# Performance work log

Measured on AMD Instinct MI355X. Metric: run time of the kernel, lower is better.

## Reference

```python
import jax, jax.numpy as jnp
import numpy as np

V = 32000   # vocab.size
E = 512     # embed_dim
H = 512     # hidden_dim
L = 2       # num_layers
W = 32      # window_size
S = 512     # seq_len
B = 8       # batch


def setup_inputs() -> dict:
    key = jax.random.key(0)
    ks = jax.random.split(key, 2 + 4 * L)
    bound = 1.0 / np.sqrt(H)
    inp = {
        "encoder_input": jax.random.randint(ks[0], (S, B), 0, V),
        "embed_table": jax.random.normal(ks[1], (V, E), jnp.float32),
    }
    for l in range(L):
        in_dim = E if l == 0 else H
        k = ks[2 + 4 * l: 6 + 4 * l]
        inp[f"w_ih_{l}"] = jax.random.uniform(k[0], (4 * H, in_dim), jnp.float32, -bound, bound)
        inp[f"w_hh_{l}"] = jax.random.uniform(k[1], (4 * H, H), jnp.float32, -bound, bound)
        inp[f"b_ih_{l}"] = jax.random.uniform(k[2], (4 * H,), jnp.float32, -bound, bound)
        inp[f"b_hh_{l}"] = jax.random.uniform(k[3], (4 * H,), jnp.float32, -bound, bound)
    return inp


def _lstm_layer(x, mask, w_ih, w_hh, b_ih, b_hh):
    # x: [T, N, D]; mask: [T, N, 1]. Masked steps keep (h, c), so every window
    # effectively starts from a zero state at its first valid position (same as
    # running a fresh LSTM on each window, torch gate order i,f,g,o).
    N = x.shape[1]
    Hd = w_hh.shape[1]
    bias = b_ih + b_hh

    def step(carry, inp_):
        h, c = carry
        xt, mt = inp_
        gates = xt @ w_ih.T + h @ w_hh.T + bias  # [N, 4H]
        i, f, g, o = jnp.split(gates, 4, axis=-1)
        i = jax.nn.sigmoid(i)
        f = jax.nn.sigmoid(f)
        g = jnp.tanh(g)
        o = jax.nn.sigmoid(o)
        c_new = f * c + i * g
        h_new = o * jnp.tanh(c_new)
        h = jnp.where(mt, h_new, h)
        c = jnp.where(mt, c_new, c)
        return (h, c), h

    z = jnp.zeros((N, Hd), x.dtype)
    (h, _), ys = jax.lax.scan(step, (z, z), (x, mask))
    return ys, h


def reference(encoder_input, embed_table,
              w_ih_0, w_hh_0, b_ih_0, b_hh_0,
              w_ih_1, w_hh_1, b_ih_1, b_hh_1):
    emb = embed_table[encoder_input]              # [S, B, E]
    T = W + 1
    # window position t for target index i is i - W + t (invalid when < 0)
    pos = jnp.arange(S)[None, :] - W + jnp.arange(T)[:, None]  # [T, S]
    valid = pos >= 0
    windows = emb[jnp.clip(pos, 0)]               # [T, S, B, E]
    x = windows.reshape(T, S * B, E)
    mask = jnp.broadcast_to(valid[:, :, None], (T, S, B)).reshape(T, S * B, 1)

    params = [(w_ih_0, w_hh_0, b_ih_0, b_hh_0), (w_ih_1, w_hh_1, b_ih_1, b_hh_1)]
    h = None
    for (wi, wh, bi, bh) in params:
        x, h = _lstm_layer(x, mask, wi, wh, bi, bh)
    # original takes encoder_output at the last window position == final hidden
    return h.reshape(S, B, H)
```

## Files before the change

### kernel.cpp

```cpp
#include <hip/hip_runtime.h>
#include <stdint.h>

#define NROWS 4096
#define HDIM  512
#define GDIM  2048
#define WWIN  32

typedef __attribute__((ext_vector_type(8))) short short8;
typedef __attribute__((ext_vector_type(4))) float f32x4;

__device__ __forceinline__ unsigned short f2bf(float x){
  union { float f; unsigned int u; } v; v.f = x;
  unsigned int u = v.u + 0x7fffu + ((v.u >> 16) & 1u);
  return (unsigned short)(u >> 16);
}
__device__ __forceinline__ float bf2f(unsigned short u){
  union { unsigned int u; float f; } v; v.u = ((unsigned int)u) << 16; return v.f;
}

__device__ __forceinline__ void gld16(const void* g, void* l){
  __builtin_amdgcn_global_load_lds(
      (const __attribute__((address_space(1))) unsigned int*)g,
      (__attribute__((address_space(3))) unsigned int*)l, 16, 0, 0);
}

__device__ __forceinline__ float sigm(float x){ return 1.f/(1.f + __expf(-x)); }
__device__ __forceinline__ float tanh_f(float x){ return 1.f - 2.f/(1.f + __expf(2.f*x)); }

__device__ __forceinline__ void grid_sync(unsigned* bar, unsigned target){
  __syncthreads();
  if (threadIdx.x == 0){
    unsigned arrived = __hip_atomic_fetch_add(&bar[0], 1u, __ATOMIC_RELAXED,
                                              __HIP_MEMORY_SCOPE_AGENT);
    if (arrived == gridDim.x - 1){
      __hip_atomic_store(&bar[0], 0u, __ATOMIC_RELAXED, __HIP_MEMORY_SCOPE_AGENT);
      __hip_atomic_store(&bar[1], target, __ATOMIC_RELAXED, __HIP_MEMORY_SCOPE_AGENT);
    } else {
      while (__hip_atomic_load(&bar[1], __ATOMIC_RELAXED, __HIP_MEMORY_SCOPE_AGENT) < target)
        __builtin_amdgcn_s_sleep(8);
    }
  }
  asm volatile("" ::: "memory");
  __syncthreads();
}

__device__ __forceinline__ void gemm_tile_db(
    const char* A0, const char* A1, const char* Bsrc,
    int ldbB, int nk, int r0, int c0,
    char* smem, int wr, int wc, int lane, f32x4 acc[4][4])
{
  const int tid = threadIdx.x;
  const int oo0 = tid * 16;
  const int srow = oo0 >> 7;
  const int scb  = oo0 & 127;
  const size_t aOff = (size_t)(r0 + srow) * 1024 + scb;
  const size_t bOff = (size_t)(c0 + srow) * (size_t)ldbB + scb;

  auto STAGE = [&](int kk, int buf){
    const char* Ap = (kk < 8) ? A0 : A1;
    const size_t kbA = (size_t)(kk & 7) * 128;
    const size_t kbB = (size_t)kk * 128;
    char* AsB = smem + buf * 16384;
    char* BsB = smem + 32768 + buf * 16384;
    #pragma unroll
    for (int i = 0; i < 4; ++i){
      const size_t rstep = (size_t)i * 32;
      gld16(Ap   + aOff + rstep * 1024          + kbA, AsB + i*4096 + oo0);
      gld16(Bsrc + bOff + rstep * (size_t)ldbB  + kbB, BsB + i*4096 + oo0);
    }
  };

  STAGE(0, 0);
  __syncthreads();

  const int lr = lane & 15;
  const int lk = (lane >> 4) * 8;

  for (int kk = 0; kk < nk; ++kk){
    const int cur = kk & 1;
    if (kk + 1 < nk) STAGE(kk + 1, cur ^ 1);

    const unsigned short* As = (const unsigned short*)(smem + cur*16384);
    const unsigned short* Bs = (const unsigned short*)(smem + 32768 + cur*16384);
    short8 a[2][4], b[2][4];
    #pragma unroll
    for (int h = 0; h < 2; ++h){
      const int k32 = h * 32;
      #pragma unroll
      for (int m = 0; m < 4; ++m)
        a[h][m] = *(const short8*)(As + (64*wr + 16*m + lr)*64 + k32 + lk);
      #pragma unroll
      for (int n = 0; n < 4; ++n)
        b[h][n] = *(const short8*)(Bs + (64*wc + 16*n + lr)*64 + k32 + lk);
    }
    __builtin_amdgcn_s_setprio(1);
    #pragma unroll
    for (int h = 0; h < 2; ++h)
      #pragma unroll
      for (int m = 0; m < 4; ++m)
        #pragma unroll
        for (int n = 0; n < 4; ++n)
          acc[m][n] = __builtin_amdgcn_mfma_f32_16x16x32_bf16(a[h][m], b[h][n], acc[m][n], 0, 0, 0);
    __builtin_amdgcn_s_setprio(0);

    __syncthreads();
  }
}

__global__ void __launch_bounds__(256) prep_weights(
    const float* wih0, const float* whh0, const float* bih0, const float* bhh0,
    const float* wih1, const float* whh1, const float* bih1, const float* bhh1,
    unsigned short* BrIh0, unsigned short* Br0, unsigned short* Br1,
    float* bias0r, float* br1)
{
  const int j = blockIdx.x;
  const int g = j & 3, hd = j >> 2;
  const int r = g*512 + hd;
  for (int k = threadIdx.x; k < 512; k += 256){
    BrIh0[(size_t)j*512 + k]      = f2bf(wih0[(size_t)r*512 + k]);
    Br0  [(size_t)j*512 + k]      = f2bf(whh0[(size_t)r*512 + k]);
    Br1  [(size_t)j*1024 + k]     = f2bf(wih1[(size_t)r*512 + k]);
    Br1  [(size_t)j*1024 + 512+k] = f2bf(whh1[(size_t)r*512 + k]);
  }
  if (threadIdx.x == 0){
    bias0r[j] = bih0[r] + bhh0[r];
    br1[j]    = bih1[r] + bhh1[r];
  }
}

__global__ void __launch_bounds__(256) gather_embed(const int* enc, const float* tbl,
                                                    unsigned short* E)
{
  const int n = blockIdx.x;
  const int idx = enc[n];
  const float* src = tbl + (size_t)idx * 512;
  unsigned short* dst = E + (size_t)n * 512;
  for (int e = threadIdx.x; e < 512; e += 256) dst[e] = f2bf(src[e]);
}

__global__ void __launch_bounds__(256) p0_gemm(const unsigned short* E,
                                               const unsigned short* BrIh0,
                                               const float* bias0r,
                                               unsigned short* P0)
{
  __shared__ __align__(16) char smem[65536];
  const int tid  = threadIdx.x;
  const int lane = tid & 63, wid = tid >> 6;
  const int wr = wid >> 1, wc = wid & 1;
  const int bid = blockIdx.x;
  const int r0 = (bid >> 4) * 128, c0 = (bid & 15) * 128;
  f32x4 acc[4][4] = {};
  gemm_tile_db((const char*)E, nullptr, (const char*)BrIh0, 1024, 8,
               r0, c0, smem, wr, wc, lane, acc);
  #pragma unroll
  for (int m = 0; m < 4; ++m){
    const int rowb = r0 + 64*wr + 16*m + ((lane >> 4) << 2);
    #pragma unroll
    for (int n = 0; n < 4; ++n){
      const int colb = c0 + 64*wc + 16*n + (lane & 15);
      const float bs = bias0r[colb];
      #pragma unroll
      for (int r = 0; r < 4; ++r)
        P0[(size_t)(rowb + r)*GDIM + colb] = f2bf(acc[m][n][r] + bs);
    }
  }
}

__global__ void __launch_bounds__(512, 2) persist_kernel(
    unsigned short* h0, unsigned short* h1,
    const unsigned short* Br0, const unsigned short* Br1,
    const unsigned short* P0, const float* br1, float* out, unsigned* bar)
{
  extern __shared__ __align__(16) char smem[];

  const int bid = blockIdx.x;
  const int x = bid & 7, i = bid >> 3;
  const bool L1 = (i & 1);
  const int rowg = (x >> 1) * 4 + ((i >> 1) & 3);
  const int colg = (x & 1) * 4 + ((i >> 3) & 3);
  const int r0  = rowg * 256;
  const int c0v = colg * 256;

  const int tid  = threadIdx.x;
  const int lane = tid & 63, wid = tid >> 6;
  const int wm = wid >> 2, wn = wid & 3;
  const int lr = lane & 15, sl = lane >> 4;
  const int ph = (sl ^ ((lr >> 1) & 3)) << 4;

  const int srowB  = tid >> 2;
  const int sbyteB = ((tid & 3) ^ ((tid >> 3) & 3)) << 4;
  const int ar   = tid >> 1;
  const int as0  = (tid & 1) * 2;
  const int akey = (ar >> 1) & 3;

  const char* Bp  = (const char*)(L1 ? Br1 : Br0);
  const int  ldbB = L1 ? 2048 : 1024;
  const int  nkt  = L1 ? 32 : 16;

  float creg[4][4][2];
  #pragma unroll
  for (int p = 0; p < 4; ++p)
    #pragma unroll
    for (int q = 0; q < 4; ++q){ creg[p][q][0] = 0.f; creg[p][q][1] = 0.f; }

  for (int tau = 0; tau <= 33; ++tau){
    const bool active = L1 ? (tau >= 1) : (tau <= 32);
    if (active){
      const int t  = L1 ? (tau - 1) : tau;
      const int pr = (tau + 1) & 1, pw = tau & 1;
      const unsigned short* hA0 = h0 + (size_t)pr * (NROWS*HDIM);
      const unsigned short* hA1 = h1 + (size_t)pr * (NROWS*HDIM);

      auto issueB = [&](int kt2){
        const char* s0 = Bp + (size_t)(c0v + srowB) * (size_t)ldbB + kt2*64 + sbyteB;
        char* d = smem + 32768 + (size_t)(kt2 & 3) * 16384 + tid * 16;
        gld16(s0, d);
        gld16(s0 + (size_t)128 * (size_t)ldbB, d + 8192);
      };
      auto issueA = [&](int kt2, unsigned long long a[4]){
        const unsigned short* hs; int kE;
        if (!L1 || kt2 < 16){ hs = hA0; kE = kt2 * 32; }
        else                { hs = hA1; kE = (kt2 - 16) * 32; }
        unsigned long long* p = (unsigned long long*)(hs + (size_t)(r0 + ar) * 512 + kE + as0 * 8);
        a[0] = __hip_atomic_load(p+0, __ATOMIC_RELAXED, __HIP_MEMORY_SCOPE_AGENT);
        a[1] = __hip_atomic_load(p+1, __ATOMIC_RELAXED, __HIP_MEMORY_SCOPE_AGENT);
        a[2] = __hip_atomic_load(p+2, __ATOMIC_RELAXED, __HIP_MEMORY_SCOPE_AGENT);
        a[3] = __hip_atomic_load(p+3, __ATOMIC_RELAXED, __HIP_MEMORY_SCOPE_AGENT);
      };
      auto writeA = [&](int kt2, const unsigned long long a[4]){
        char* base = smem + (size_t)(kt2 & 1) * 16384 + ar * 64;
        char* p0 = base + ((as0 ^ akey) << 4);
        char* p1 = base + (((as0 + 1) ^ akey) << 4);
        *(unsigned long long*)(p0)     = a[0];
        *(unsigned long long*)(p0 + 8) = a[1];
        *(unsigned long long*)(p1)     = a[2];
        *(unsigned long long*)(p1 + 8) = a[3];
      };

      f32x4 acc[8][4] = {};
      unsigned long long areg[4];

      issueA(0, areg);
      issueB(0); issueB(1);
      asm volatile("s_waitcnt vmcnt(4)" ::: "memory");
      writeA(0, areg);
      issueA(1, areg);
      asm volatile("s_waitcnt vmcnt(4)" ::: "memory");
      asm volatile("s_waitcnt lgkmcnt(0)" ::: "memory");
      __builtin_amdgcn_s_barrier();

      for (int kt = 0; kt < nkt; ++kt){
        const char* Ab = smem + (size_t)(kt & 1) * 16384;
        const char* Bb = smem + 32768 + (size_t)(kt & 3) * 16384;
        short8 a[8], b[4];
        #pragma unroll
        for (int m = 0; m < 8; ++m)
          a[m] = *(const short8*)(Ab + (wm*128 + m*16 + lr)*64 + ph);
        #pragma unroll
        for (int n = 0; n < 4; ++n)
          b[n] = *(const short8*)(Bb + (wn*64 + n*16 + lr)*64 + ph);

        const bool stB = (kt + 2) < nkt;
        if (stB) issueB(kt + 2);

        __builtin_amdgcn_s_setprio(1);
        #pragma unroll
        for (int m = 0; m < 8; ++m)
          #pragma unroll
          for (int n = 0; n < 4; ++n)
            acc[m][n] = __builtin_amdgcn_mfma_f32_16x16x32_bf16(a[m], b[n], acc[m][n], 0, 0, 0);
        __builtin_amdgcn_s_setprio(0);

        if (stB) asm volatile("s_waitcnt vmcnt(2)" ::: "memory");
        else     asm volatile("s_waitcnt vmcnt(0)" ::: "memory");
        if (kt + 1 < nkt){
          writeA(kt + 1, areg);
          if (kt + 2 < nkt) issueA(kt + 2, areg);
        }
        asm volatile("s_waitcnt lgkmcnt(0)" ::: "memory");
        __builtin_amdgcn_s_barrier();
      }

      float* GLDS = (float*)smem;
      const int GST = 68;
      unsigned short* hw = (L1 ? h1 : h0) + (size_t)pw * (NROWS*HDIM);
      const bool finalStep = (L1 && t == 32);
      const int cbase = c0v >> 2;

      #pragma unroll
      for (int pass = 0; pass < 4; ++pass){
        __syncthreads();
        if (wn == pass){
          #pragma unroll
          for (int m = 0; m < 8; ++m){
            const int rowb = wm*128 + m*16 + (sl << 2);
            #pragma unroll
            for (int n = 0; n < 4; ++n){
              const int colb = n*16 + lr;
              const f32x4 v = acc[m][n];
              #pragma unroll
              for (int r = 0; r < 4; ++r)
                GLDS[(rowb + r)*GST + colb] = v[r];
            }
          }
        }
        __syncthreads();
        #pragma unroll
        for (int it = 0; it < 4; ++it){
          const int pid = it*512 + tid;
          const int row = pid >> 3;
          const int pl  = (pid & 7) * 2;
          const int rowg = r0 + row;
          const int hd0  = cbase + pass*16 + pl;
          const float* gp = &GLDS[row*GST + 4*pl];
          const float4 g0 = *(const float4*)gp;
          const float4 g1 = *(const float4*)(gp + 4);
          float gi0 = g0.x, gf0 = g0.y, gg0 = g0.z, go0 = g0.w;
          float gi1 = g1.x, gf1 = g1.y, gg1 = g1.z, go1 = g1.w;
          const int s  = rowg >> 3;
          const int bb = rowg & 7;
          const int pos = s - WWIN + t;
          if (!L1){
            const int p0r = (pos < 0 ? 0 : pos)*8 + bb;
            const uint4 pv = *(const uint4*)&P0[(size_t)p0r*GDIM + 4*hd0];
            gi0 += bf2f((unsigned short)(pv.x & 0xffff));
            gf0 += bf2f((unsigned short)(pv.x >> 16));
            gg0 += bf2f((unsigned short)(pv.y & 0xffff));
            go0 += bf2f((unsigned short)(pv.y >> 16));
            gi1 += bf2f((unsigned short)(pv.z & 0xffff));
            gf1 += bf2f((unsigned short)(pv.z >> 16));
            gg1 += bf2f((unsigned short)(pv.w & 0xffff));
            go1 += bf2f((unsigned short)(pv.w >> 16));
          } else {
            const float4 b0 = *(const float4*)&br1[4*hd0];
            const float4 b1 = *(const float4*)&br1[4*hd0 + 4];
            gi0 += b0.x; gf0 += b0.y; gg0 += b0.z; go0 += b0.w;
            gi1 += b1.x; gf1 += b1.y; gg1 += b1.z; go1 += b1.w;
          }
          float cp0 = creg[pass][it][0];
          float cp1 = creg[pass][it][1];
          float i0 = sigm(gi0), f0 = sigm(gf0), gA = tanh_f(gg0), o0 = sigm(go0);
          float i1 = sigm(gi1), f1 = sigm(gf1), gB = tanh_f(gg1), o1 = sigm(go1);
          float cn0 = f0*cp0 + i0*gA;
          float cn1 = f1*cp1 + i1*gB;
          float hn0 = o0*tanh_f(cn0);
          float hn1 = o1*tanh_f(cn1);
          if (pos < 0){ cn0 = 0.f; hn0 = 0.f; cn1 = 0.f; hn1 = 0.f; }
          creg[pass][it][0] = cn0;
          creg[pass][it][1] = cn1;
          const size_t sidx0 = (size_t)rowg*HDIM + hd0;
          if (finalStep){
            *(float2*)&out[sidx0] = make_float2(hn0, hn1);
          } else {
            const unsigned hp = (unsigned)f2bf(hn0) | ((unsigned)f2bf(hn1) << 16);
            __hip_atomic_store((unsigned*)&hw[sidx0], hp, __ATOMIC_RELAXED,
                               __HIP_MEMORY_SCOPE_AGENT);
          }
        }
      }
    }
    if (tau != 33) grid_sync(bar, (unsigned)(tau + 1));
  }
}

__global__ void __launch_bounds__(512, 2) step_kernel(
    unsigned short* h0, unsigned short* h1, float* c0b, float* c1b,
    const unsigned short* Br0, const unsigned short* Br1,
    const unsigned short* P0, const float* br1, float* out, int tau, int bidOff)
{
  extern __shared__ __align__(16) char smem[];

  const int x = blockIdx.x & 7, kq = blockIdx.x >> 3;
  int wk;
  if (gridDim.x == 256) wk = ((kq & 1) << 7) + x * 16 + (kq >> 1);
  else                  wk = x * 16 + kq;
  wk += bidOff;

  const bool L1 = (wk >= 128);
  const int t  = L1 ? (tau - 1) : tau;
  const int pr = (tau + 1) & 1, pw = tau & 1;
  const int lb = L1 ? (wk - 128) : wk;
  const int r0  = (lb >> 3) * 256;
  const int c0v = (lb & 7) * 256;

  const int tid  = threadIdx.x;
  const int lane = tid & 63;
  const int wid  = tid >> 6;
  const int wm = wid >> 2, wn = wid & 3;
  const int lr = lane & 15, sl = lane >> 4;

  const unsigned short* hA0 = h0 + (size_t)pr * (NROWS*HDIM);
  const unsigned short* hA1 = h1 + (size_t)pr * (NROWS*HDIM);
  const char* Bp  = (const char*)(L1 ? Br1 : Br0);
  const int  ldbB = L1 ? 2048 : 1024;
  const int  nkt  = L1 ? 32 : 16;

  const int srow  = tid >> 2;
  const int sbyte = ((tid & 3) ^ ((tid >> 3) & 3)) << 4;
  const int ph    = (sl ^ ((lr >> 1) & 3)) << 4;
  const int laneA = (wm*128 + lr) * 64 + ph;
  const int laneB = (wn*64  + lr) * 64 + ph;

  auto STAGE_A = [&](int kt2, int c){
    const char* Ap; int kB;
    if (!L1 || kt2 < 16){ Ap = (const char*)hA0; kB = kt2 * 64; }
    else                { Ap = (const char*)hA1; kB = (kt2 - 16) * 64; }
    gld16(Ap + (size_t)(r0 + c*128 + srow) * 1024 + kB + sbyte,
          smem + (size_t)(kt2 & 3) * 32768 + c*8192 + tid*16);
  };
  auto STAGE_B = [&](int kt2, int c){
    gld16(Bp + (size_t)(c0v + c*128 + srow) * (size_t)ldbB + kt2*64 + sbyte,
          smem + (size_t)(kt2 & 3) * 32768 + 16384 + c*8192 + tid*16);
  };

  f32x4 acc[8][4] = {};

  STAGE_A(0,0); STAGE_A(0,1); STAGE_B(0,0); STAGE_B(0,1);
  STAGE_A(1,0); STAGE_A(1,1); STAGE_B(1,0); STAGE_B(1,1);
  asm volatile("s_waitcnt vmcnt(4)" ::: "memory");
  __builtin_amdgcn_s_barrier();

  for (int kt = 0; kt < nkt; ++kt){
    const char* bufp = smem + (size_t)(kt & 3) * 32768;
    const bool st = (kt + 2) < nkt;
    short8 a0[4], a1[4], b[4];

    #pragma unroll
    for (int m = 0; m < 4; ++m) a0[m] = *(const short8*)(bufp + laneA + m*1024);
    #pragma unroll
    for (int n = 0; n < 4; ++n) b[n]  = *(const short8*)(bufp + 16384 + laneB + n*1024);
    if (st){ STAGE_A(kt+2, 0); STAGE_A(kt+2, 1); }
    __builtin_amdgcn_s_barrier();
    asm volatile("s_waitcnt lgkmcnt(0)" ::: "memory");
    __builtin_amdgcn_sched_barrier(0);
    __builtin_amdgcn_s_setprio(1);
    #pragma unroll
    for (int m = 0; m < 4; ++m)
      #pragma unroll
      for (int n = 0; n < 4; ++n)
        acc[m][n] = __builtin_amdgcn_mfma_f32_16x16x32_bf16(a0[m], b[n], acc[m][n], 0, 0, 0);
    __builtin_amdgcn_s_setprio(0);
    __builtin_amdgcn_s_barrier();

    #pragma unroll
    for (int m = 0; m < 4; ++m) a1[m] = *(const short8*)(bufp + laneA + (4+m)*1024);
    if (st){
      STAGE_B(kt+2, 0); STAGE_B(kt+2, 1);
      asm volatile("s_waitcnt vmcnt(4)" ::: "memory");
    } else {
      asm volatile("s_waitcnt vmcnt(0)" ::: "memory");
    }
    __builtin_amdgcn_s_barrier();
    asm volatile("s_waitcnt lgkmcnt(0)" ::: "memory");
    __builtin_amdgcn_sched_barrier(0);
    __builtin_amdgcn_s_setprio(1);
    #pragma unroll
    for (int m = 0; m < 4; ++m)
      #pragma unroll
      for (int n = 0; n < 4; ++n)
        acc[4+m][n] = __builtin_amdgcn_mfma_f32_16x16x32_bf16(a1[m], b[n], acc[4+m][n], 0, 0, 0);
    __builtin_amdgcn_s_setprio(0);
    __builtin_amdgcn_s_barrier();
  }

  float* GLDS = (float*)smem;
  const int GST = 68;
  float* cbuf = L1 ? c1b : c0b;
  unsigned short* hw = (L1 ? h1 : h0) + (size_t)pw * (NROWS*HDIM);
  const bool finalStep = (L1 && t == 32);

  for (int pass = 0; pass < 4; ++pass){
    __syncthreads();
    if (wn == pass){
      #pragma unroll
      for (int m = 0; m < 8; ++m){
        const int rowb = wm*128 + m*16 + (sl << 2);
        #pragma unroll
        for (int n = 0; n < 4; ++n){
          const int colb = n*16 + lr;
          const f32x4 v = acc[m][n];
          #pragma unroll
          for (int r = 0; r < 4; ++r)
            GLDS[(rowb + r)*GST + colb] = v[r];
        }
      }
    }
    __syncthreads();
    #pragma unroll
    for (int it = 0; it < 8; ++it){
      const int cid = it*512 + tid;
      const int row = cid >> 4;
      const int l   = cid & 15;
      const int rowg = r0 + row;
      const int hd   = (c0v >> 2) + pass*16 + l;
      float4 gv = *(const float4*)&GLDS[row*GST + 4*l];
      float gi = gv.x, gf = gv.y, gg = gv.z, go = gv.w;
      const int s  = rowg >> 3;
      const int bb = rowg & 7;
      const int pos = s - WWIN + t;
      if (!L1){
        const int p0r = (pos < 0 ? 0 : pos)*8 + bb;
        const ushort4 pv = *(const ushort4*)&P0[(size_t)p0r*GDIM + 4*hd];
        gi += bf2f(pv.x); gf += bf2f(pv.y); gg += bf2f(pv.z); go += bf2f(pv.w);
      } else {
        float4 bv = *(const float4*)&br1[4*hd];
        gi += bv.x; gf += bv.y; gg += bv.z; go += bv.w;
      }
      const size_t sidx = (size_t)rowg*HDIM + hd;
      float cp = cbuf[sidx];
      float i_ = sigm(gi), f_ = sigm(gf), g_ = tanh_f(gg), o_ = sigm(go);
      float cn = f_*cp + i_*g_;
      float hn = o_*tanh_f(cn);
      if (pos < 0){ cn = 0.f; hn = 0.f; }
      cbuf[sidx] = cn;
      if (finalStep) out[sidx] = hn;
      else           hw[sidx]  = f2bf(hn);
    }
  }
}

extern "C" void kernel_launch(void* const* d_in, const int* in_sizes, int n_in,
                              void* d_out, int out_size, void* d_ws, size_t ws_size,
                              hipStream_t stream)
{
  const int*   enc  = (const int*)d_in[0];
  const float* tbl  = (const float*)d_in[1];
  const float* wih0 = (const float*)d_in[2];
  const float* whh0 = (const float*)d_in[3];
  const float* bih0 = (const float*)d_in[4];
  const float* bhh0 = (const float*)d_in[5];
  const float* wih1 = (const float*)d_in[6];
  const float* whh1 = (const float*)d_in[7];
  const float* bih1 = (const float*)d_in[8];
  const float* bhh1 = (const float*)d_in[9];
  float* out = (float*)d_out;

  char* ws = (char*)d_ws;
  size_t off = 0;
  auto alloc = [&](size_t bytes){
    char* p = ws + off; off += (bytes + 255) & ~(size_t)255; return p;
  };
  unsigned short* E     = (unsigned short*)alloc((size_t)NROWS*512*2);
  unsigned short* BrIh0 = (unsigned short*)alloc((size_t)GDIM*512*2);
  unsigned short* Br0   = (unsigned short*)alloc((size_t)GDIM*512*2);
  unsigned short* Br1   = (unsigned short*)alloc((size_t)GDIM*1024*2);
  float* bias0r = (float*)alloc(GDIM*4);
  float* br1    = (float*)alloc(GDIM*4);
  unsigned short* P0 = (unsigned short*)alloc((size_t)NROWS*GDIM*2);
  unsigned short* h0 = (unsigned short*)alloc((size_t)2*NROWS*HDIM*2);
  unsigned short* h1 = (unsigned short*)alloc((size_t)2*NROWS*HDIM*2);
  float* c0 = (float*)alloc((size_t)NROWS*HDIM*4);
  float* c1 = (float*)alloc((size_t)NROWS*HDIM*4);
  unsigned* bar = (unsigned*)alloc(256);
  if (off > ws_size) return;

  (void)hipFuncSetAttribute(reinterpret_cast<const void*>(persist_kernel),
                            hipFuncAttributeMaxDynamicSharedMemorySize, 98304);
  (void)hipFuncSetAttribute(reinterpret_cast<const void*>(step_kernel),
                            hipFuncAttributeMaxDynamicSharedMemorySize, 131072);

  hipMemsetAsync(h0, 0, (size_t)33554688, stream);

  prep_weights<<<2048, 256, 0, stream>>>(wih0, whh0, bih0, bhh0,
                                         wih1, whh1, bih1, bhh1,
                                         BrIh0, Br0, Br1, bias0r, br1);
  gather_embed<<<4096, 256, 0, stream>>>(enc, tbl, E);
  p0_gemm<<<512, 256, 0, stream>>>(E, BrIh0, bias0r, P0);

  int occ = 0;
  hipError_t oe = hipOccupancyMaxActiveBlocksPerMultiprocessor(
      &occ, reinterpret_cast<const void*>(persist_kernel), 512, 98304);
  bool coop = (oe == hipSuccess && occ >= 1);
  if (coop){
    void* kargs[] = {&h0, &h1, &Br0, &Br1, &P0, &br1, &out, &bar};
    hipError_t le = hipLaunchCooperativeKernel(
        reinterpret_cast<const void*>(persist_kernel),
        dim3(256), dim3(512), kargs, 98304, stream);
    if (le != hipSuccess) coop = false;
  }
  if (!coop){
    for (int tau = 0; tau <= 33; ++tau){
      const int grid = (tau == 0 || tau == 33) ? 128 : 256;
      const int boff = (tau == 33) ? 128 : 0;
      step_kernel<<<grid, 512, 131072, stream>>>(h0, h1, c0, c1, Br0, Br1,
                                                 P0, br1, out, tau, boff);
    }
  }
}
```

Measured before the change: 1.739 ms.

## Split persistent LSTM grid into 512 smaller blocks with per-row-band barriers

The persistent kernel now launches 512 blocks of 256 threads, each owning a 128-row by 256-column tile instead of 256-row by 256-column tiles, with smaller LDS buffers. The global grid barrier is replaced by a counter per 128-row band, so only the 16 blocks that share a band of hidden rows wait for each other at each timestep. This is meant to cut barrier latency and use more CUs for the recurrent GEMM. In exchange, B-matrix tiles go from triple-buffered to double-buffered and each block does more loads per unit of compute. The cooperative launch path also now requires an occupancy of 2 blocks per CU.

Measured after the change: 1.738 ms. Within noise of the previous version (-0.1%).

```diff
diff --git a/kernel.cpp b/kernel.cpp
--- a/kernel.cpp
+++ b/kernel.cpp
@@ -27,18 +27,12 @@
 __device__ __forceinline__ float sigm(float x){ return 1.f/(1.f + __expf(-x)); }
 __device__ __forceinline__ float tanh_f(float x){ return 1.f - 2.f/(1.f + __expf(2.f*x)); }
 
-__device__ __forceinline__ void grid_sync(unsigned* bar, unsigned target){
+__device__ __forceinline__ void band_sync(unsigned* ctr, unsigned target){
   __syncthreads();
   if (threadIdx.x == 0){
-    unsigned arrived = __hip_atomic_fetch_add(&bar[0], 1u, __ATOMIC_RELAXED,
-                                              __HIP_MEMORY_SCOPE_AGENT);
-    if (arrived == gridDim.x - 1){
-      __hip_atomic_store(&bar[0], 0u, __ATOMIC_RELAXED, __HIP_MEMORY_SCOPE_AGENT);
-      __hip_atomic_store(&bar[1], target, __ATOMIC_RELAXED, __HIP_MEMORY_SCOPE_AGENT);
-    } else {
-      while (__hip_atomic_load(&bar[1], __ATOMIC_RELAXED, __HIP_MEMORY_SCOPE_AGENT) < target)
-        __builtin_amdgcn_s_sleep(8);
-    }
+    __hip_atomic_fetch_add(ctr, 1u, __ATOMIC_RELAXED, __HIP_MEMORY_SCOPE_AGENT);
+    while (__hip_atomic_load(ctr, __ATOMIC_RELAXED, __HIP_MEMORY_SCOPE_AGENT) < target)
+      __builtin_amdgcn_s_sleep(2);
   }
   asm volatile("" ::: "memory");
   __syncthreads();
@@ -166,28 +160,27 @@
   }
 }
 
-__global__ void __launch_bounds__(512, 2) persist_kernel(
+__global__ void __launch_bounds__(256, 2) persist_kernel(
     unsigned short* h0, unsigned short* h1,
     const unsigned short* Br0, const unsigned short* Br1,
     const unsigned short* P0, const float* br1, float* out, unsigned* bar)
 {
   extern __shared__ __align__(16) char smem[];
 
-  const int bid = blockIdx.x;
-  const int x = bid & 7, i = bid >> 3;
-  const bool L1 = (i & 1);
-  const int rowg = (x >> 1) * 4 + ((i >> 1) & 3);
-  const int colg = (x & 1) * 4 + ((i >> 3) & 3);
-  const int r0  = rowg * 256;
-  const int c0v = colg * 256;
+  const int bid  = blockIdx.x;
+  const int colg = bid & 7;
+  const int bl   = bid >> 3;
+  const bool L1  = (bl & 1);
+  const int rb   = bl >> 1;
+  const int r0   = rb * 128;
+  const int c0v  = colg * 256;
 
   const int tid  = threadIdx.x;
   const int lane = tid & 63, wid = tid >> 6;
-  const int wm = wid >> 2, wn = wid & 3;
+  const int wn = wid;
   const int lr = lane & 15, sl = lane >> 4;
   const int ph = (sl ^ ((lr >> 1) & 3)) << 4;
 
-  const int srowB  = tid >> 2;
   const int sbyteB = ((tid & 3) ^ ((tid >> 3) & 3)) << 4;
   const int ar   = tid >> 1;
   const int as0  = (tid & 1) * 2;
@@ -196,6 +189,8 @@
   const char* Bp  = (const char*)(L1 ? Br1 : Br0);
   const int  ldbB = L1 ? 2048 : 1024;
   const int  nkt  = L1 ? 32 : 16;
+
+  unsigned* ctr = bar + rb * 32;
 
   float creg[4][4][2];
   #pragma unroll
@@ -212,23 +207,26 @@
       const unsigned short* hA1 = h1 + (size_t)pr * (NROWS*HDIM);
 
       auto issueB = [&](int kt2){
-        const char* s0 = Bp + (size_t)(c0v + srowB) * (size_t)ldbB + kt2*64 + sbyteB;
-        char* d = smem + 32768 + (size_t)(kt2 & 3) * 16384 + tid * 16;
-        gld16(s0, d);
-        gld16(s0 + (size_t)128 * (size_t)ldbB, d + 8192);
+        char* d = smem + 16384 + (size_t)(kt2 & 1) * 16384 + tid * 16;
+        const char* s = Bp + (size_t)(c0v + (tid >> 2)) * (size_t)ldbB
+                           + kt2 * 64 + sbyteB;
+        #pragma unroll
+        for (int i = 0; i < 4; ++i)
+          gld16(s + (size_t)(i * 64) * (size_t)ldbB, d + i * 4096);
       };
       auto issueA = [&](int kt2, unsigned long long a[4]){
         const unsigned short* hs; int kE;
         if (!L1 || kt2 < 16){ hs = hA0; kE = kt2 * 32; }
         else                { hs = hA1; kE = (kt2 - 16) * 32; }
-        unsigned long long* p = (unsigned long long*)(hs + (size_t)(r0 + ar) * 512 + kE + as0 * 8);
+        const unsigned long long* p =
+            (const unsigned long long*)(hs + (size_t)(r0 + ar) * 512 + kE + as0 * 8);
         a[0] = __hip_atomic_load(p+0, __ATOMIC_RELAXED, __HIP_MEMORY_SCOPE_AGENT);
         a[1] = __hip_atomic_load(p+1, __ATOMIC_RELAXED, __HIP_MEMORY_SCOPE_AGENT);
         a[2] = __hip_atomic_load(p+2, __ATOMIC_RELAXED, __HIP_MEMORY_SCOPE_AGENT);
         a[3] = __hip_atomic_load(p+3, __ATOMIC_RELAXED, __HIP_MEMORY_SCOPE_AGENT);
       };
       auto writeA = [&](int kt2, const unsigned long long a[4]){
-        char* base = smem + (size_t)(kt2 & 1) * 16384 + ar * 64;
+        char* base = smem + (size_t)(kt2 & 1) * 8192 + ar * 64;
         char* p0 = base + ((as0 ^ akey) << 4);
         char* p1 = base + (((as0 + 1) ^ akey) << 4);
         *(unsigned long long*)(p0)     = a[0];
@@ -241,8 +239,7 @@
       unsigned long long areg[4];
 
       issueA(0, areg);
-      issueB(0); issueB(1);
-      asm volatile("s_waitcnt vmcnt(4)" ::: "memory");
+      issueB(0);
       writeA(0, areg);
       issueA(1, areg);
       asm volatile("s_waitcnt vmcnt(4)" ::: "memory");
@@ -250,18 +247,16 @@
       __builtin_amdgcn_s_barrier();
 
       for (int kt = 0; kt < nkt; ++kt){
-        const char* Ab = smem + (size_t)(kt & 1) * 16384;
-        const char* Bb = smem + 32768 + (size_t)(kt & 3) * 16384;
+        if (kt + 1 < nkt) issueB(kt + 1);
+        const char* Ab = smem + (size_t)(kt & 1) * 8192;
+        const char* Bb = smem + 16384 + (size_t)(kt & 1) * 16384;
         short8 a[8], b[4];
-        #pragma unroll
-        for (int m = 0; m < 8; ++m)
-          a[m] = *(const short8*)(Ab + (wm*128 + m*16 + lr)*64 + ph);
         #pragma unroll
         for (int n = 0; n < 4; ++n)
           b[n] = *(const short8*)(Bb + (wn*64 + n*16 + lr)*64 + ph);
-
-        const bool stB = (kt + 2) < nkt;
-        if (stB) issueB(kt + 2);
+        #pragma unroll
+        for (int m = 0; m < 8; ++m)
+          a[m] = *(const short8*)(Ab + (m*16 + lr)*64 + ph);
 
         __builtin_amdgcn_s_setprio(1);
         #pragma unroll
@@ -271,14 +266,17 @@
             acc[m][n] = __builtin_amdgcn_mfma_f32_16x16x32_bf16(a[m], b[n], acc[m][n], 0, 0, 0);
         __builtin_amdgcn_s_setprio(0);
 
-        if (stB) asm volatile("s_waitcnt vmcnt(2)" ::: "memory");
-        else     asm volatile("s_waitcnt vmcnt(0)" ::: "memory");
         if (kt + 1 < nkt){
           writeA(kt + 1, areg);
-          if (kt + 2 < nkt) issueA(kt + 2, areg);
+          if (kt + 2 < nkt){
+            issueA(kt + 2, areg);
+            asm volatile("s_waitcnt vmcnt(4)" ::: "memory");
+          } else {
+            asm volatile("s_waitcnt vmcnt(0)" ::: "memory");
+          }
+          asm volatile("s_waitcnt lgkmcnt(0)" ::: "memory");
+          __builtin_amdgcn_s_barrier();
         }
-        asm volatile("s_waitcnt lgkmcnt(0)" ::: "memory");
-        __builtin_amdgcn_s_barrier();
       }
 
       float* GLDS = (float*)smem;
@@ -293,7 +291,7 @@
         if (wn == pass){
           #pragma unroll
           for (int m = 0; m < 8; ++m){
-            const int rowb = wm*128 + m*16 + (sl << 2);
+            const int rowb = m*16 + (sl << 2);
             #pragma unroll
             for (int n = 0; n < 4; ++n){
               const int colb = n*16 + lr;
@@ -307,7 +305,7 @@
         __syncthreads();
         #pragma unroll
         for (int it = 0; it < 4; ++it){
-          const int pid = it*512 + tid;
+          const int pid = it*256 + tid;
           const int row = pid >> 3;
           const int pl  = (pid & 7) * 2;
           const int rowg = r0 + row;
@@ -359,7 +357,7 @@
         }
       }
     }
-    if (tau != 33) grid_sync(bar, (unsigned)(tau + 1));
+    if (tau != 33) band_sync(ctr, 16u * (unsigned)(tau + 1));
   }
 }
 
@@ -551,15 +549,15 @@
   unsigned short* h1 = (unsigned short*)alloc((size_t)2*NROWS*HDIM*2);
   float* c0 = (float*)alloc((size_t)NROWS*HDIM*4);
   float* c1 = (float*)alloc((size_t)NROWS*HDIM*4);
-  unsigned* bar = (unsigned*)alloc(256);
+  unsigned* bar = (unsigned*)alloc(4096);
   if (off > ws_size) return;
 
   (void)hipFuncSetAttribute(reinterpret_cast<const void*>(persist_kernel),
-                            hipFuncAttributeMaxDynamicSharedMemorySize, 98304);
+                            hipFuncAttributeMaxDynamicSharedMemorySize, 65536);
   (void)hipFuncSetAttribute(reinterpret_cast<const void*>(step_kernel),
                             hipFuncAttributeMaxDynamicSharedMemorySize, 131072);
 
-  hipMemsetAsync(h0, 0, (size_t)33554688, stream);
+  hipMemsetAsync(h0, 0, (size_t)33558528, stream);
 
   prep_weights<<<2048, 256, 0, stream>>>(wih0, whh0, bih0, bhh0,
                                          wih1, whh1, bih1, bhh1,
@@ -569,13 +567,13 @@
 
   int occ = 0;
   hipError_t oe = hipOccupancyMaxActiveBlocksPerMultiprocessor(
-      &occ, reinterpret_cast<const void*>(persist_kernel), 512, 98304);
-  bool coop = (oe == hipSuccess && occ >= 1);
+      &occ, reinterpret_cast<const void*>(persist_kernel), 256, 49152);
+  bool coop = (oe == hipSuccess && occ >= 2);
   if (coop){
     void* kargs[] = {&h0, &h1, &Br0, &Br1, &P0, &br1, &out, &bar};
     hipError_t le = hipLaunchCooperativeKernel(
         reinterpret_cast<const void*>(persist_kernel),
-        dim3(256), dim3(512), kargs, 98304, stream);
+        dim3(512), dim3(256), kargs, 49152, stream);
     if (le != hipSuccess) coop = false;
   }
   if (!coop){
```
